# Kernel optimization log

Measured on AMD Instinct MI355X. Metric: run time of the kernel, lower is better.

The kernel has to match this reference:

```python
import jax, jax.numpy as jnp
import numpy as np

B, N, C, H = 2, 2048, 1024, 16
D = C // H          # head_dim = 64
HALF = D // 2       # 32 complex pairs per head


def setup_inputs() -> dict:
    key = jax.random.key(0)
    k1, k2, k3, k4 = jax.random.split(key, 4)
    x = jax.random.normal(k1, (B, N, C), dtype=jnp.float32)
    # 0.02 init scale keeps softmax logits in a sane range
    qkv_w = jax.random.normal(k2, (3 * C, C), dtype=jnp.float32) * 0.02
    proj_w = jax.random.normal(k3, (C, C), dtype=jnp.float32) * 0.02
    proj_b = jax.random.normal(k4, (C,), dtype=jnp.float32) * 0.02
    # standard RoPE frequencies: theta = 10000^{-2i/D}
    inv_freq = 1.0 / (10000.0 ** (jnp.arange(0, D, 2, dtype=jnp.float32) / D))
    angles = jnp.arange(N, dtype=jnp.float32)[:, None] * inv_freq[None, :]  # [N, HALF]
    return {
        "x": x, "qkv_w": qkv_w, "proj_w": proj_w, "proj_b": proj_b,
        "freqs_cos": jnp.cos(angles), "freqs_sin": jnp.sin(angles),
    }


def _rope(t, cos, sin):
    # t: [B, N, H, D]; cos/sin: [N, HALF] -> broadcast as [1, N, 1, HALF]
    tr = t.reshape(B, N, H, HALF, 2)
    t_re, t_im = tr[..., 0], tr[..., 1]
    c = cos[None, :, None, :]
    s = sin[None, :, None, :]
    o_re = t_re * c - t_im * s
    o_im = t_re * s + t_im * c
    return jnp.stack([o_re, o_im], axis=-1).reshape(B, N, H, D)


def reference(x, qkv_w, proj_w, proj_b, freqs_cos, freqs_sin):
    scale = D ** -0.5
    qkv = x @ qkv_w.T                              # [B, N, 3C] (no bias: qkv_bias=False)
    qkv = qkv.reshape(B, N, 3, H, D)
    q, k, v = qkv[:, :, 0], qkv[:, :, 1], qkv[:, :, 2]  # [B, N, H, D]
    q = _rope(q, freqs_cos, freqs_sin)
    k = _rope(k, freqs_cos, freqs_sin)
    scores = jnp.einsum("bqhd,bkhd->bhqk", q, k) * scale
    attn = jax.nn.softmax(scores, axis=-1)         # dropout p=0.0 -> identity
    out = jnp.einsum("bhqk,bkhd->bqhd", attn, v).reshape(B, N, C)
    return out @ proj_w.T + proj_b
```

## Files before the change

### kernel.cpp

```cpp
#include <hip/hip_runtime.h>
#include <hip/hip_bf16.h>

#define B_ 2
#define N_ 2048
#define C_ 1024
#define H_ 16
#define D_ 64
#define HALF_ 32

typedef __attribute__((ext_vector_type(8))) __bf16 bf16x8;
typedef __attribute__((ext_vector_type(8))) unsigned short u16x8;
typedef __attribute__((ext_vector_type(4))) float f32x4;
typedef __attribute__((ext_vector_type(16))) float f32x16;

__device__ __forceinline__ unsigned short f2bf(float f) {
  union { float f; unsigned u; } v; v.f = f;
  unsigned r = v.u + 0x7FFFu + ((v.u >> 16) & 1u);
  return (unsigned short)(r >> 16);
}

__device__ __forceinline__ unsigned cvt_pk_bf16(float lo, float hi) {
  unsigned r;
  asm("v_cvt_pk_bf16_f32 %0, %1, %2" : "=v"(r) : "v"(lo), "v"(hi));
  return r;
}

__device__ __forceinline__ void gload_lds16(const void* g, void* l) {
  __builtin_amdgcn_global_load_lds(
      (const __attribute__((address_space(1))) void*)g,
      (__attribute__((address_space(3))) void*)l, 16, 0, 0);
}

__global__ __launch_bounds__(256) void cast3_f32_bf16(
    const float* __restrict__ a, const float* __restrict__ b,
    const float* __restrict__ c, unsigned short* __restrict__ oa,
    unsigned short* __restrict__ ob, unsigned short* __restrict__ oc,
    const float* __restrict__ cosT, const float* __restrict__ sinT,
    float2* __restrict__ csT) {
  int i = blockIdx.x * 256 + threadIdx.x;
  if (i >= 2097152) {
    int i2 = i - 2097152;
    csT[i2] = make_float2(cosT[i2], sinT[i2]);
    return;
  }
  const float4* src;
  ushort4* dst;
  int off;
  if (i < 1048576) {
    src = (const float4*)a; dst = (ushort4*)oa; off = i;
  } else if (i < 1835008) {
    src = (const float4*)b; dst = (ushort4*)ob; off = i - 1048576;
  } else {
    src = (const float4*)c; dst = (ushort4*)oc; off = i - 1835008;
  }
  float4 v = src[off];
  ushort4 o;
  o.x = f2bf(v.x); o.y = f2bf(v.y); o.z = f2bf(v.z); o.w = f2bf(v.w);
  dst[off] = o;
}

template <int EPI>
__global__ __launch_bounds__(256) void gemm_bt(
    const unsigned short* __restrict__ A, const unsigned short* __restrict__ Bw,
    int M, int Nn, int K,
    float* __restrict__ Cout, const float* __restrict__ bias,
    unsigned short* __restrict__ qo, unsigned short* __restrict__ ko,
    unsigned short* __restrict__ vto,
    const float2* __restrict__ csT) {
  __shared__ __align__(16) unsigned short As[2][128][64];
  __shared__ __align__(16) unsigned short Bs[2][128][64];
  const int tid = threadIdx.x;
  const int lane = tid & 63;
  const int wid = tid >> 6;
  const int wm = wid >> 1, wn = wid & 1;
  const int l15 = lane & 15;
  const int g = lane >> 4;

  const int per = gridDim.x >> 3;
  const int f = blockIdx.x;
  const int nat = (f & 7) * per + (f >> 3);
  const int mtiles = M >> 7;
  const int m0 = (nat % mtiles) * 128;
  const int n0 = (nat / mtiles) * 128;

  const int srow = wid * 8 + (lane >> 3);
  const int scol = (lane & 7) * 8;

  auto stage = [&](int kt, int buf) {
#pragma unroll
    for (int j = 0; j < 4; ++j) {
      gload_lds16(&A[(size_t)(m0 + j * 32 + srow) * K + kt * 64 + scol],
                  &As[buf][j * 32 + wid * 8][0]);
      gload_lds16(&Bw[(size_t)(n0 + j * 32 + srow) * K + kt * 64 + scol],
                  &Bs[buf][j * 32 + wid * 8][0]);
    }
  };

  f32x4 acc[4][4] = {};

  const int nK = K >> 6;
  stage(0, 0);
  stage(1, 1);

  for (int kt = 0; kt < nK; ++kt) {
    const int buf = kt & 1;
    if (kt == nK - 1) asm volatile("s_waitcnt vmcnt(0)" ::: "memory");
    else              asm volatile("s_waitcnt vmcnt(8)" ::: "memory");
    __builtin_amdgcn_s_barrier();
    __builtin_amdgcn_sched_barrier(0);
#pragma unroll
    for (int kk = 0; kk < 2; ++kk) {
      bf16x8 af[4], bfv[4];
#pragma unroll
      for (int m = 0; m < 4; ++m)
        af[m] = *reinterpret_cast<const bf16x8*>(&As[buf][wm * 64 + m * 16 + l15][kk * 32 + g * 8]);
#pragma unroll
      for (int n = 0; n < 4; ++n)
        bfv[n] = *reinterpret_cast<const bf16x8*>(&Bs[buf][wn * 64 + n * 16 + l15][kk * 32 + g * 8]);
#pragma unroll
      for (int m = 0; m < 4; ++m)
#pragma unroll
        for (int n = 0; n < 4; ++n)
          acc[m][n] = __builtin_amdgcn_mfma_f32_16x16x32_bf16(af[m], bfv[n], acc[m][n], 0, 0, 0);
    }
    __builtin_amdgcn_s_barrier();
    if (kt + 2 < nK) stage(kt + 2, buf);
  }

  if constexpr (EPI == 0) {
#pragma unroll
    for (int n = 0; n < 4; ++n) {
      int col = n0 + wn * 64 + n * 16 + l15;
      float bv = bias[col];
#pragma unroll
      for (int m = 0; m < 4; ++m) {
        int rbase = m0 + wm * 64 + m * 16 + g * 4;
#pragma unroll
        for (int r = 0; r < 4; ++r)
          Cout[(size_t)(rbase + r) * Nn + col] = acc[m][n][r] + bv;
      }
    }
  } else {
    const int which = n0 >> 10;
    if (which == 2) {
#pragma unroll
      for (int m = 0; m < 4; ++m)
#pragma unroll
        for (int n = 0; n < 4; ++n) {
          int col = n0 + wn * 64 + n * 16 + l15;
          int hc = col & 1023;
          int hh = hc >> 6, d = hc & 63;
          int row0 = m0 + wm * 64 + m * 16 + g * 4;
          int seq0 = row0 & (N_ - 1), bb = row0 >> 11;
          int seqP = (seq0 & ~12) | ((seq0 & 4) << 1) | ((seq0 & 8) >> 1);
          ushort4 pk;
          pk.x = f2bf(acc[m][n][0]); pk.y = f2bf(acc[m][n][1]);
          pk.z = f2bf(acc[m][n][2]); pk.w = f2bf(acc[m][n][3]);
          *reinterpret_cast<ushort4*>(
              &vto[(((size_t)bb * H_ + hh) * D_ + d) * N_ + seqP]) = pk;
        }
    } else {
      unsigned short* dst = (which == 0) ? qo : ko;
      const float qscale = (which == 0) ? 0.125f * 1.44269504f : 1.0f;
#pragma unroll
      for (int m = 0; m < 4; ++m)
#pragma unroll
        for (int n = 0; n < 4; ++n)
#pragma unroll
          for (int r = 0; r < 4; ++r) {
            int col = n0 + wn * 64 + n * 16 + l15;
            int row = m0 + wm * 64 + m * 16 + g * 4 + r;
            float val = acc[m][n][r];
            float partner = __shfl_xor(val, 1);
            int hc = col & 1023;
            int hh = hc >> 6, d = hc & 63;
            int seq = row & (N_ - 1), bb = row >> 11;
            float2 cs = csT[seq * HALF_ + (d >> 1)];
            float res = (d & 1) ? (partner * cs.y + val * cs.x) : (val * cs.x - partner * cs.y);
            res *= qscale;
            dst[(((size_t)bb * H_ + hh) * N_ + seq) * D_ + d] = f2bf(res);
          }
    }
  }
}

__global__ __launch_bounds__(512) void attn_kernel(
    const unsigned short* __restrict__ q,
    const unsigned short* __restrict__ k,
    const unsigned short* __restrict__ vt,
    unsigned short* __restrict__ o) {
  __shared__ __align__(16) unsigned short Kl[2][64][64];
  __shared__ __align__(16) unsigned short Vl[2][64][64];

  const int tid = threadIdx.x;
  const int lane = tid & 63;
  const int w = tid >> 6;
  const int l31 = lane & 31;
  const int hi = lane >> 5;

  const int bid = blockIdx.x;
  const int nat = (bid & 7) * 32 + (bid >> 3);
  const int qt = nat & 7;
  const int bh = nat >> 3;
  const int b = bh >> 4, h = bh & 15;

  const size_t hk = (size_t)bh * N_ * D_;
  const size_t hv = (size_t)bh * D_ * N_;
  const int qrow = qt * 256 + w * 32 + l31;

  bf16x8 qf[4];
#pragma unroll
  for (int kt = 0; kt < 4; ++kt)
    qf[kt] = *reinterpret_cast<const bf16x8*>(
        &q[hk + (size_t)qrow * D_ + kt * 16 + hi * 8]);

  const int prow = tid >> 3;
  const int pchk = tid & 7;
  const int swz = (pchk ^ (prow & 7)) * 8;

  u16x8 kr, vr;
  auto issueK = [&](int t) {
    kr = *reinterpret_cast<const u16x8*>(&k[hk + (size_t)(t * 64 + prow) * D_ + pchk * 8]);
  };
  auto issueV = [&](int t) {
    vr = *reinterpret_cast<const u16x8*>(&vt[hv + (size_t)prow * N_ + t * 64 + pchk * 8]);
  };
  auto commitK = [&](int buf) { *reinterpret_cast<u16x8*>(&Kl[buf][prow][swz]) = kr; };
  auto commitV = [&](int buf) { *reinterpret_cast<u16x8*>(&Vl[buf][prow][swz]) = vr; };

  f32x16 accO[2] = {};
  float lrun = 0.f;
  const int b7 = l31 & 7;
  const int NT = N_ / 64;

  f32x16 sA[2], sB[2];

#define QK_MFMA(T, SC)                                                        \
  do {                                                                        \
    f32x16 z_ = {};                                                           \
    SC[0] = z_; SC[1] = z_;                                                   \
    __builtin_amdgcn_s_setprio(1);                                            \
    _Pragma("unroll")                                                         \
    for (int kb = 0; kb < 2; ++kb)                                            \
      _Pragma("unroll")                                                       \
      for (int kt = 0; kt < 4; ++kt) {                                        \
        bf16x8 kf = *reinterpret_cast<const bf16x8*>(                         \
            &Kl[(T) & 1][kb * 32 + l31][(((kt * 2 + hi) ^ b7)) * 8]);         \
        SC[kb] = __builtin_amdgcn_mfma_f32_32x32x16_bf16(kf, qf[kt], SC[kb], 0, 0, 0); \
      }                                                                       \
    __builtin_amdgcn_s_setprio(0);                                            \
  } while (0)

#define SMPV(SP, VB)                                                          \
  do {                                                                        \
    _Pragma("unroll")                                                         \
    for (int kb = 0; kb < 2; ++kb)                                            \
      _Pragma("unroll")                                                       \
      for (int i = 0; i < 16; ++i) SP[kb][i] = __builtin_exp2f(SP[kb][i]);    \
    float sloc[16];                                                           \
    _Pragma("unroll")                                                         \
    for (int i = 0; i < 16; ++i) sloc[i] = SP[0][i] + SP[1][i];               \
    _Pragma("unroll")                                                         \
    for (int st = 8; st > 0; st >>= 1)                                        \
      _Pragma("unroll")                                                       \
      for (int i = 0; i < 8; ++i)                                             \
        if (i < st) sloc[i] += sloc[i + st];                                  \
    {                                                                         \
      unsigned ua = __float_as_uint(sloc[0]), ub = ua;                        \
      auto rr = __builtin_amdgcn_permlane32_swap(ua, ub, false, false);       \
      lrun += __uint_as_float(rr[0]) + __uint_as_float(rr[1]);                \
    }                                                                         \
    bf16x8 PA[4];                                                             \
    _Pragma("unroll")                                                         \
    for (int kvc = 0; kvc < 4; ++kvc) {                                       \
      const int kb = kvc >> 1, base = (kvc & 1) * 8;                          \
      union { unsigned u[4]; bf16x8 v; } pa;                                  \
      _Pragma("unroll")                                                       \
      for (int wd = 0; wd < 4; ++wd)                                          \
        pa.u[wd] = cvt_pk_bf16(SP[kb][base + 2 * wd], SP[kb][base + 2 * wd + 1]); \
      PA[kvc] = pa.v;                                                         \
    }                                                                         \
    __builtin_amdgcn_s_setprio(1);                                            \
    _Pragma("unroll")                                                         \
    for (int db = 0; db < 2; ++db)                                            \
      _Pragma("unroll")                                                       \
      for (int kvc = 0; kvc < 4; ++kvc) {                                     \
        bf16x8 vf = *reinterpret_cast<const bf16x8*>(                         \
            &Vl[VB][db * 32 + l31][(((kvc * 2 + hi) ^ b7)) * 8]);             \
        accO[db] = __builtin_amdgcn_mfma_f32_32x32x16_bf16(vf, PA[kvc], accO[db], 0, 0, 0); \
      }                                                                       \
    __builtin_amdgcn_s_setprio(0);                                            \
  } while (0)

#define BODY(T, SP, SC)                                                       \
  do {                                                                        \
    const int t_ = (T);                                                       \
    if (t_ + 1 < NT) issueK(t_ + 1);                                          \
    issueV(t_);                                                               \
    QK_MFMA(t_, SC);                                                          \
    SMPV(SP, (t_ - 1) & 1);                                                   \
    if (t_ + 1 < NT) commitK((t_ + 1) & 1);                                   \
    commitV(t_ & 1);                                                          \
    __syncthreads();                                                          \
  } while (0)

  issueK(0);
  commitK(0);
  __syncthreads();

  issueK(1);
  issueV(0);
  QK_MFMA(0, sA);
  commitK(1);
  commitV(0);
  __syncthreads();

  for (int tt = 1; tt + 1 < NT; tt += 2) {
    BODY(tt, sA, sB);
    BODY(tt + 1, sB, sA);
  }
  BODY(NT - 1, sA, sB);

  SMPV(sB, (NT - 1) & 1);

  float rl = 1.0f / lrun;
  const size_t obase = ((size_t)b * N_ + qrow) * C_ + h * 64;
#pragma unroll
  for (int db = 0; db < 2; ++db)
#pragma unroll
    for (int rg = 0; rg < 4; ++rg) {
      ushort4 pk;
      pk.x = f2bf(accO[db][rg * 4 + 0] * rl);
      pk.y = f2bf(accO[db][rg * 4 + 1] * rl);
      pk.z = f2bf(accO[db][rg * 4 + 2] * rl);
      pk.w = f2bf(accO[db][rg * 4 + 3] * rl);
      *reinterpret_cast<ushort4*>(&o[obase + db * 32 + rg * 8 + hi * 4]) = pk;
    }
#undef BODY
#undef SMPV
#undef QK_MFMA
}

extern "C" void kernel_launch(void* const* d_in, const int* in_sizes, int n_in,
                              void* d_out, int out_size, void* d_ws, size_t ws_size,
                              hipStream_t stream) {
  const float* x      = (const float*)d_in[0];
  const float* qkv_w  = (const float*)d_in[1];
  const float* proj_w = (const float*)d_in[2];
  const float* proj_b = (const float*)d_in[3];
  const float* cosT   = (const float*)d_in[4];
  const float* sinT   = (const float*)d_in[5];
  float* out = (float*)d_out;

  unsigned short* xb     = (unsigned short*)d_ws;
  unsigned short* wqkvb  = xb + (size_t)4096 * 1024;
  unsigned short* wprojb = wqkvb + (size_t)3072 * 1024;
  unsigned short* qb     = wprojb + (size_t)1024 * 1024;
  unsigned short* kb     = qb + (size_t)32 * 2048 * 64;
  unsigned short* vtb    = kb + (size_t)32 * 2048 * 64;
  unsigned short* ab     = vtb + (size_t)32 * 2048 * 64;
  float2* csT            = (float2*)(ab + (size_t)4096 * 1024);

  cast3_f32_bf16<<<8448, 256, 0, stream>>>(x, qkv_w, proj_w, xb, wqkvb, wprojb,
                                           cosT, sinT, csT);

  gemm_bt<1><<<768, 256, 0, stream>>>(xb, wqkvb, 4096, 3072, 1024,
                                      nullptr, nullptr, qb, kb, vtb, csT);

  attn_kernel<<<256, 512, 0, stream>>>(qb, kb, vtb, ab);

  gemm_bt<0><<<256, 256, 0, stream>>>(ab, wprojb, 4096, 1024, 1024,
                                      out, proj_b, nullptr, nullptr, nullptr,
                                      csT);
}
```

Baseline: 141.3 us.

## Use smaller attention blocks, pair RoPE stores, fold accumulator zeroing into MFMA

The attention kernel moves from 256 blocks of 512 threads, each covering 256 query rows, to 512 blocks of 256 threads covering 128 rows. Each thread now loads two K/V rows per tile. The aim is to spread work over more CUs (256 CUs on MI355X) and to shrink per-block size. The cost is that each K/V tile is loaded twice as often across blocks. The RoPE epilogue in the QKV GEMM now has only even lanes compute both halves of a rotation pair and write them as one packed 32-bit bf16 store. The QK MFMA takes a zero accumulator on its first k-step instead of clearing the registers beforehand.

New measurement: 166.8 us. +18.1%, slower.

```diff
diff --git a/kernel.cpp b/kernel.cpp
--- a/kernel.cpp
+++ b/kernel.cpp
@@ -170,21 +170,25 @@
           for (int r = 0; r < 4; ++r) {
             int col = n0 + wn * 64 + n * 16 + l15;
             int row = m0 + wm * 64 + m * 16 + g * 4 + r;
-            float val = acc[m][n][r];
-            float partner = __shfl_xor(val, 1);
-            int hc = col & 1023;
-            int hh = hc >> 6, d = hc & 63;
-            int seq = row & (N_ - 1), bb = row >> 11;
-            float2 cs = csT[seq * HALF_ + (d >> 1)];
-            float res = (d & 1) ? (partner * cs.y + val * cs.x) : (val * cs.x - partner * cs.y);
-            res *= qscale;
-            dst[(((size_t)bb * H_ + hh) * N_ + seq) * D_ + d] = f2bf(res);
+            float re = acc[m][n][r];
+            float im = __shfl_xor(re, 1);
+            if (!(l15 & 1)) {
+              int hc = col & 1023;
+              int hh = hc >> 6, d = hc & 63;
+              int seq = row & (N_ - 1), bb = row >> 11;
+              float2 cs = csT[seq * HALF_ + (d >> 1)];
+              float re2 = (re * cs.x - im * cs.y) * qscale;
+              float im2 = (re * cs.y + im * cs.x) * qscale;
+              *reinterpret_cast<unsigned*>(
+                  &dst[(((size_t)bb * H_ + hh) * N_ + seq) * D_ + d]) =
+                  cvt_pk_bf16(re2, im2);
+            }
           }
     }
   }
 }
 
-__global__ __launch_bounds__(512) void attn_kernel(
+__global__ __launch_bounds__(256) void attn_kernel(
     const unsigned short* __restrict__ q,
     const unsigned short* __restrict__ k,
     const unsigned short* __restrict__ vt,
@@ -199,14 +203,14 @@
   const int hi = lane >> 5;
 
   const int bid = blockIdx.x;
-  const int nat = (bid & 7) * 32 + (bid >> 3);
-  const int qt = nat & 7;
-  const int bh = nat >> 3;
+  const int nat = (bid & 7) * 64 + (bid >> 3);
+  const int qt = nat & 15;
+  const int bh = nat >> 4;
   const int b = bh >> 4, h = bh & 15;
 
   const size_t hk = (size_t)bh * N_ * D_;
   const size_t hv = (size_t)bh * D_ * N_;
-  const int qrow = qt * 256 + w * 32 + l31;
+  const int qrow = qt * 128 + w * 32 + l31;
 
   bf16x8 qf[4];
 #pragma unroll
@@ -218,27 +222,34 @@
   const int pchk = tid & 7;
   const int swz = (pchk ^ (prow & 7)) * 8;
 
-  u16x8 kr, vr;
+  u16x8 kr0, kr1, vr0, vr1;
   auto issueK = [&](int t) {
-    kr = *reinterpret_cast<const u16x8*>(&k[hk + (size_t)(t * 64 + prow) * D_ + pchk * 8]);
+    kr0 = *reinterpret_cast<const u16x8*>(&k[hk + (size_t)(t * 64 + prow) * D_ + pchk * 8]);
+    kr1 = *reinterpret_cast<const u16x8*>(&k[hk + (size_t)(t * 64 + prow + 32) * D_ + pchk * 8]);
   };
   auto issueV = [&](int t) {
-    vr = *reinterpret_cast<const u16x8*>(&vt[hv + (size_t)prow * N_ + t * 64 + pchk * 8]);
-  };
-  auto commitK = [&](int buf) { *reinterpret_cast<u16x8*>(&Kl[buf][prow][swz]) = kr; };
-  auto commitV = [&](int buf) { *reinterpret_cast<u16x8*>(&Vl[buf][prow][swz]) = vr; };
+    vr0 = *reinterpret_cast<const u16x8*>(&vt[hv + (size_t)prow * N_ + t * 64 + pchk * 8]);
+    vr1 = *reinterpret_cast<const u16x8*>(&vt[hv + (size_t)(prow + 32) * N_ + t * 64 + pchk * 8]);
+  };
+  auto commitK = [&](int buf) {
+    *reinterpret_cast<u16x8*>(&Kl[buf][prow][swz]) = kr0;
+    *reinterpret_cast<u16x8*>(&Kl[buf][prow + 32][swz]) = kr1;
+  };
+  auto commitV = [&](int buf) {
+    *reinterpret_cast<u16x8*>(&Vl[buf][prow][swz]) = vr0;
+    *reinterpret_cast<u16x8*>(&Vl[buf][prow + 32][swz]) = vr1;
+  };
 
   f32x16 accO[2] = {};
   float lrun = 0.f;
   const int b7 = l31 & 7;
   const int NT = N_ / 64;
+  const f32x16 FZERO = {};
 
   f32x16 sA[2], sB[2];
 
 #define QK_MFMA(T, SC)                                                        \
   do {                                                                        \
-    f32x16 z_ = {};                                                           \
-    SC[0] = z_; SC[1] = z_;                                                   \
     __builtin_amdgcn_s_setprio(1);                                            \
     _Pragma("unroll")                                                         \
     for (int kb = 0; kb < 2; ++kb)                                            \
@@ -246,7 +257,8 @@
       for (int kt = 0; kt < 4; ++kt) {                                        \
         bf16x8 kf = *reinterpret_cast<const bf16x8*>(                         \
             &Kl[(T) & 1][kb * 32 + l31][(((kt * 2 + hi) ^ b7)) * 8]);         \
-        SC[kb] = __builtin_amdgcn_mfma_f32_32x32x16_bf16(kf, qf[kt], SC[kb], 0, 0, 0); \
+        SC[kb] = __builtin_amdgcn_mfma_f32_32x32x16_bf16(                     \
+            kf, qf[kt], (kt == 0) ? FZERO : SC[kb], 0, 0, 0);                 \
       }                                                                       \
     __builtin_amdgcn_s_setprio(0);                                            \
   } while (0)
@@ -367,7 +379,7 @@
   gemm_bt<1><<<768, 256, 0, stream>>>(xb, wqkvb, 4096, 3072, 1024,
                                       nullptr, nullptr, qb, kb, vtb, csT);
 
-  attn_kernel<<<256, 512, 0, stream>>>(qb, kb, vtb, ab);
+  attn_kernel<<<512, 256, 0, stream>>>(qb, kb, vtb, ab);
 
   gemm_bt<0><<<256, 256, 0, stream>>>(ab, wprojb, 4096, 1024, 1024,
                                       out, proj_b, nullptr, nullptr, nullptr,
```
